# Optimization experiments

Measured on AMD Instinct MI355X. Metric: run time of the kernel, lower is better.

The kernel has to match this reference:

```python
import jax, jax.numpy as jnp
import numpy as np
import math

B, C, IMG, P = 256, 3, 32, 4
D, H = 256, 8
HD = D // H
T = (IMG // P) ** 2          # 64 patches
T1 = T + 1                   # +cls token
MLP_H = 2048
HEAD_H = T * D // 2          # 8192
NUM_CLASSES = 10
PATCH_DIM = C * P * P


def _pe(t1, d):
    pos = jnp.arange(t1, dtype=jnp.float32)[:, None]
    div = jnp.exp(jnp.arange(0, d, 2, dtype=jnp.float32) * (-math.log(10000.0) / d))
    s = jnp.sin(pos * div)   # [T1, d/2]
    c = jnp.cos(pos * div)
    return jnp.stack([s, c], axis=-1).reshape(t1, d)  # interleave: even=sin, odd=cos


def _ln2d(x, w, b, eps=1e-5):
    # LayerNorm over last two dims [T1, D] with affine params of shape [T1, D]
    mu = jnp.mean(x, axis=(-2, -1), keepdims=True)
    var = jnp.mean((x - mu) ** 2, axis=(-2, -1), keepdims=True)
    return (x - mu) * jax.lax.rsqrt(var + eps) * w + b


def setup_inputs() -> dict:
    key = jax.random.key(0)
    ks = jax.random.split(key, 16)
    s = 0.02
    inp = {
        "x": jax.random.normal(ks[0], (B, C, IMG, IMG), dtype=jnp.float32),
        "cls_token": jax.random.normal(ks[1], (1, 1, D), dtype=jnp.float32),
        "Wp": jax.random.normal(ks[2], (PATCH_DIM, D), dtype=jnp.float32) * s,
        "bp": jnp.zeros((D,), jnp.float32),
        # 2 transformer blocks, params stacked on leading axis
        "qkv_w": jax.random.normal(ks[3], (2, D, 3 * D), dtype=jnp.float32) * s,
        "qkv_b": jnp.zeros((2, 3 * D), jnp.float32),
        "ln_w": jnp.ones((2, T1, D), jnp.float32),
        "ln_b": jnp.zeros((2, T1, D), jnp.float32),
        "mlp1_w": jax.random.normal(ks[4], (2, D, MLP_H), dtype=jnp.float32) * s,
        "mlp1_b": jnp.zeros((2, MLP_H), jnp.float32),
        "mlp2_w": jax.random.normal(ks[5], (2, MLP_H, D), dtype=jnp.float32) * s,
        "mlp2_b": jnp.zeros((2, D), jnp.float32),
        "head1_w": jax.random.normal(ks[6], (T1 * D, HEAD_H), dtype=jnp.float32) * s,
        "head1_b": jnp.zeros((HEAD_H,), jnp.float32),
        "head2_w": jax.random.normal(ks[7], (HEAD_H, NUM_CLASSES), dtype=jnp.float32) * s,
        "head2_b": jnp.zeros((NUM_CLASSES,), jnp.float32),
    }
    return inp


def reference(x, cls_token, Wp, bp, qkv_w, qkv_b, ln_w, ln_b,
              mlp1_w, mlp1_b, mlp2_w, mlp2_b, head1_w, head1_b, head2_w, head2_b):
    b = x.shape[0]
    n = IMG // P
    # patchify: [B,C,n,P,n,P] -> [B,n,n,C,P,P] -> [B, T, C*P*P]  (C-major per patch)
    patches = x.reshape(b, C, n, P, n, P).transpose(0, 2, 4, 1, 3, 5).reshape(b, T, PATCH_DIM)
    out = patches @ Wp + bp                                     # [B, T, D]
    cls = jnp.broadcast_to(cls_token, (b, 1, D))
    out = jnp.concatenate([cls, out], axis=1)                   # [B, T1, D]
    out = out + _pe(T1, D)[None]

    scale = 1.0 / math.sqrt(HD)
    for i in range(2):  # dropout is eval-mode identity
        h = _ln2d(out, ln_w[i], ln_b[i])
        qkv = (h @ qkv_w[i] + qkv_b[i]).reshape(b, T1, H, 3, HD)
        q, k, v = qkv[..., 0, :], qkv[..., 1, :], qkv[..., 2, :]   # [B,S,H,hd]
        scores = jnp.einsum('bqhd,bkhd->bhqk', q, k) * scale
        a = jax.nn.softmax(scores, axis=-1)
        attn = jnp.einsum('bhqk,bkhd->bqhd', a, v).reshape(b, T1, D)
        r = attn + out
        h2 = _ln2d(r, ln_w[i], ln_b[i])                          # same LN reused
        m = jax.nn.relu(h2 @ mlp1_w[i] + mlp1_b[i])
        out = (m @ mlp2_w[i] + mlp2_b[i]) + r

    flat = out.reshape(b, T1 * D)
    hidden = jax.nn.silu(flat @ head1_w + head1_b)
    return hidden @ head2_w + head2_b                            # [B, 10] logits
```

## Files before the change

kernel.cpp:

```cpp
#include <hip/hip_runtime.h>
#include <hip/hip_fp16.h>
#include <math.h>
#include <stdint.h>

#define B_ 256
#define C_ 3
#define IMG_ 32
#define D_ 256
#define H_ 8
#define HD_ 32
#define T1_ 65
#define MLP_H_ 2048
#define HEAD_H_ 8192
#define NCLS 10
#define PDIM 48
#define M_ROWS (B_*T1_)

typedef _Float16 f16;
typedef _Float16 f16x8 __attribute__((ext_vector_type(8)));
typedef _Float16 f16x4 __attribute__((ext_vector_type(4)));
typedef float f32x4 __attribute__((ext_vector_type(4)));

typedef const void __attribute__((address_space(1))) glob_cv;
typedef void __attribute__((address_space(3))) lds_v;

__device__ __forceinline__ void async16(const void* g, void* l) {
    __builtin_amdgcn_global_load_lds((glob_cv*)g, (lds_v*)l, 16, 0, 0);
}

__global__ __launch_bounds__(256) void wpt_build(const float* __restrict__ Wp,
                                                 f16* __restrict__ WpT) {
    int idx = blockIdx.x * 256 + threadIdx.x;
    int d = idx >> 6, j = idx & 63;
    WpT[idx] = (j < PDIM) ? (f16)Wp[j * D_ + d] : (f16)0.f;
}

__global__ __launch_bounds__(256) void patch_mfma(
        const float* __restrict__ x, const float* __restrict__ cls,
        const f16* __restrict__ WpT, const float* __restrict__ bp,
        float* __restrict__ out) {
    int b = blockIdx.x;
    __shared__ float xs[3072];
    __shared__ __align__(16) f16 Ap[64 * 64];
    __shared__ __align__(16) f16 Bp[256 * 64];
    int tid = threadIdx.x;
    int lane = tid & 63, wid = tid >> 6;
    int lr = lane & 15, kq = lane >> 4;

    for (int i = tid; i < 768; i += 256)
        ((float4*)xs)[i] = ((const float4*)(x + (size_t)b * 3072))[i];
    for (int i = tid; i < 2048; i += 256)
        async16(WpT + (size_t)i * 8, &Bp[i * 8]);
    __syncthreads();
    for (int i = tid; i < 64 * 64; i += 256) {
        int t = i >> 6, j = i & 63;
        float val = 0.f;
        if (j < PDIM) {
            int py = t >> 3, px = t & 7;
            int c = j >> 4, rr = j & 15;
            int iy = rr >> 2, ix = rr & 3;
            val = xs[c * 1024 + (py * 4 + iy) * 32 + px * 4 + ix];
        }
        Ap[i] = (f16)val;
    }
    __syncthreads();

    for (int tile = wid; tile < 64; tile += 4) {
        int mi = tile >> 4, ni = tile & 15;
        f32x4 acc = {0.f, 0.f, 0.f, 0.f};
        #pragma unroll
        for (int ks = 0; ks < 2; ++ks) {
            f16x8 a = *(const f16x8*)&Ap[(mi * 16 + lr) * 64 + ks * 32 + kq * 8];
            f16x8 bb = *(const f16x8*)&Bp[(ni * 16 + lr) * 64 + ks * 32 + kq * 8];
            acc = __builtin_amdgcn_mfma_f32_16x16x32_f16(a, bb, acc, 0, 0, 0);
        }
        int d = ni * 16 + lr;
        float div = __expf((float)(d & ~1) * (-9.210340371976184f / 256.0f));
        #pragma unroll
        for (int r = 0; r < 4; ++r) {
            int t = 1 + mi * 16 + kq * 4 + r;
            float ang = (float)t * div;
            float pe = (d & 1) ? __cosf(ang) : __sinf(ang);
            out[((size_t)b * T1_ + t) * D_ + d] = acc[r] + bp[d] + pe;
        }
    }
    out[(size_t)b * T1_ * D_ + tid] = cls[tid] + ((tid & 1) ? 1.f : 0.f);
}

__global__ __launch_bounds__(1024) void ln_kernel(
        const float* __restrict__ xin, const float* __restrict__ w,
        const float* __restrict__ bb, f16* __restrict__ hout) {
    int b = blockIdx.x;
    const float4* x4 = (const float4*)(xin + (size_t)b * (T1_ * D_));
    const float4* w4 = (const float4*)w;
    const float4* b4 = (const float4*)bb;
    int tid = threadIdx.x;
    float s = 0.f, s2 = 0.f;
    for (int i = tid; i < 4160; i += 1024) {
        float4 v = x4[i];
        s  += v.x + v.y + v.z + v.w;
        s2 += v.x * v.x + v.y * v.y + v.z * v.z + v.w * v.w;
    }
    #pragma unroll
    for (int o = 32; o > 0; o >>= 1) { s += __shfl_down(s, o); s2 += __shfl_down(s2, o); }
    __shared__ float rs[16], rs2[16];
    __shared__ float mu_s, rstd_s;
    int wid = tid >> 6;
    if ((tid & 63) == 0) { rs[wid] = s; rs2[wid] = s2; }
    __syncthreads();
    if (tid == 0) {
        float S = 0.f, S2 = 0.f;
        #pragma unroll
        for (int i = 0; i < 16; ++i) { S += rs[i]; S2 += rs2[i]; }
        const float inv_n = 1.0f / (float)(T1_ * D_);
        float mu = S * inv_n;
        float var = S2 * inv_n - mu * mu;
        mu_s = mu; rstd_s = rsqrtf(var + 1e-5f);
    }
    __syncthreads();
    float mu = mu_s, rstd = rstd_s;
    f16* hb = hout + (size_t)b * (T1_ * D_);
    for (int i = tid; i < 4160; i += 1024) {
        float4 v = x4[i]; float4 wv = w4[i]; float4 bv = b4[i];
        f16x4 h;
        h[0] = (f16)((v.x - mu) * rstd * wv.x + bv.x);
        h[1] = (f16)((v.y - mu) * rstd * wv.y + bv.y);
        h[2] = (f16)((v.z - mu) * rstd * wv.z + bv.z);
        h[3] = (f16)((v.w - mu) * rstd * wv.w + bv.w);
        *(f16x4*)(hb + i * 4) = h;
    }
}

__global__ __launch_bounds__(256) void transpose_cvt(
        const float* __restrict__ W, f16* __restrict__ Wt, int K, int N) {
    __shared__ float L[32][33];
    int n0 = blockIdx.x * 32, k0 = blockIdx.y * 32;
    int t = threadIdx.x;
    int r = t >> 3, c4 = (t & 7) * 4;
    const float4 v = *(const float4*)(W + (size_t)(k0 + r) * N + n0 + c4);
    L[r][c4] = v.x; L[r][c4 + 1] = v.y; L[r][c4 + 2] = v.z; L[r][c4 + 3] = v.w;
    __syncthreads();
    f16x4 h;
    h[0] = (f16)L[c4][r]; h[1] = (f16)L[c4 + 1][r];
    h[2] = (f16)L[c4 + 2][r]; h[3] = (f16)L[c4 + 3][r];
    *(f16x4*)(Wt + (size_t)(n0 + r) * K + k0 + c4) = h;
}

template<int EPI, typename OutT>
__global__ __launch_bounds__(256) void gemm_f16(
        const f16* __restrict__ A, const f16* __restrict__ Bt,
        const float* __restrict__ bias, const float* __restrict__ Res,
        OutT* __restrict__ Cc, f16* __restrict__ C2, int M, int N, int K) {
    __shared__ __align__(16) f16 As[128 * 32];
    __shared__ __align__(16) f16 Bs[128 * 32];
    int nb = blockIdx.x, mb = blockIdx.y;
    int t = threadIdx.x;
    int lane = t & 63, wid = t >> 6;
    int wr = wid >> 1, wc = wid & 1;
    int lr = lane & 15, kq = lane >> 4;
    int row0 = mb * 128, col0 = nb * 128;

    f32x4 acc[4][4];
    #pragma unroll
    for (int mi = 0; mi < 4; ++mi)
        #pragma unroll
        for (int ni = 0; ni < 4; ++ni)
            #pragma unroll
            for (int r = 0; r < 4; ++r) acc[mi][ni][r] = 0.f;

    int sr = t >> 2;
    int k8 = (t & 3) * 8;
    const f16* Ab = A + (size_t)row0 * K + k8;
    const f16* Bb = Bt + (size_t)col0 * K + k8;

    for (int k0 = 0; k0 < K; k0 += 32) {
        __syncthreads();
        async16(Ab + (size_t)sr * K + k0,        &As[t * 8]);
        async16(Ab + (size_t)(sr + 64) * K + k0, &As[2048 + t * 8]);
        async16(Bb + (size_t)sr * K + k0,        &Bs[t * 8]);
        async16(Bb + (size_t)(sr + 64) * K + k0, &Bs[2048 + t * 8]);
        __syncthreads();
        f16x8 af[4], bf[4];
        #pragma unroll
        for (int mi = 0; mi < 4; ++mi)
            af[mi] = *(const f16x8*)&As[(wr * 64 + mi * 16 + lr) * 32 + kq * 8];
        #pragma unroll
        for (int ni = 0; ni < 4; ++ni)
            bf[ni] = *(const f16x8*)&Bs[(wc * 64 + ni * 16 + lr) * 32 + kq * 8];
        #pragma unroll
        for (int mi = 0; mi < 4; ++mi)
            #pragma unroll
            for (int ni = 0; ni < 4; ++ni)
                acc[mi][ni] = __builtin_amdgcn_mfma_f32_16x16x32_f16(af[mi], bf[ni], acc[mi][ni], 0, 0, 0);
    }

    #pragma unroll
    for (int mi = 0; mi < 4; ++mi) {
        #pragma unroll
        for (int ni = 0; ni < 4; ++ni) {
            int col = col0 + wc * 64 + ni * 16 + lr;
            #pragma unroll
            for (int r = 0; r < 4; ++r) {
                int row = row0 + wr * 64 + mi * 16 + kq * 4 + r;
                float v = acc[mi][ni][r] + bias[col];
                if (EPI == 1) v = fmaxf(v, 0.f);
                if (EPI == 2 || EPI == 3) v += Res[(size_t)row * N + col];
                Cc[(size_t)row * N + col] = (OutT)v;
                if (EPI == 3) C2[(size_t)row * N + col] = (f16)v;
            }
        }
    }
}

__global__ __launch_bounds__(256) void gemm_head1(
        const f16* __restrict__ A, const float* __restrict__ Bw,
        float* __restrict__ Cp) {
    __shared__ __align__(16) f16 As[256 * 32];
    __shared__ __align__(16) float Bs[32 * 64];
    const int K = M_ROWS, N = HEAD_H_;
    int nb = blockIdx.x;
    int z = blockIdx.y;
    int t = threadIdx.x;
    int lane = t & 63, wid = t >> 6;
    int lr = lane & 15, kq = lane >> 4;
    int col0 = nb * 64;
    int kstart = z * (K / 4);

    f32x4 acc[4][4];
    #pragma unroll
    for (int mi = 0; mi < 4; ++mi)
        #pragma unroll
        for (int ni = 0; ni < 4; ++ni)
            #pragma unroll
            for (int r = 0; r < 4; ++r) acc[mi][ni][r] = 0.f;

    int sr = t >> 2;
    int k8 = (t & 3) * 8;
    const f16* Ab = A + k8;
    int bkr = t >> 4;
    int bnc = (t & 15) * 4;
    const float* Bb = Bw + col0 + bnc;

    for (int k0 = kstart; k0 < kstart + K / 4; k0 += 32) {
        __syncthreads();
        #pragma unroll
        for (int r = 0; r < 4; ++r)
            async16(Ab + (size_t)(sr + r * 64) * K + k0, &As[r * 2048 + t * 8]);
        async16(Bb + (size_t)(k0 + bkr) * N,      &Bs[t * 4]);
        async16(Bb + (size_t)(k0 + 16 + bkr) * N, &Bs[1024 + t * 4]);
        __syncthreads();
        f16x8 af[4];
        #pragma unroll
        for (int mi = 0; mi < 4; ++mi)
            af[mi] = *(const f16x8*)&As[(wid * 64 + mi * 16 + lr) * 32 + kq * 8];
        #pragma unroll
        for (int ni = 0; ni < 4; ++ni) {
            f16x8 bf;
            #pragma unroll
            for (int j = 0; j < 8; ++j) bf[j] = (f16)Bs[(kq * 8 + j) * 64 + ni * 16 + lr];
            #pragma unroll
            for (int mi = 0; mi < 4; ++mi)
                acc[mi][ni] = __builtin_amdgcn_mfma_f32_16x16x32_f16(af[mi], bf, acc[mi][ni], 0, 0, 0);
        }
    }

    float* Cout = Cp + (size_t)z * 256 * N;
    #pragma unroll
    for (int mi = 0; mi < 4; ++mi) {
        #pragma unroll
        for (int ni = 0; ni < 4; ++ni) {
            int col = col0 + ni * 16 + lr;
            #pragma unroll
            for (int r = 0; r < 4; ++r) {
                int row = wid * 64 + mi * 16 + kq * 4 + r;
                Cout[(size_t)row * N + col] = acc[mi][ni][r];
            }
        }
    }
}

__global__ __launch_bounds__(256) void attn_kernel(
        const f16* __restrict__ qkv, const float* __restrict__ outres,
        float* __restrict__ r) {
    int b = blockIdx.x >> 3, h = blockIdx.x & 7;
    __shared__ __align__(16) f16 Qs[80 * 32];
    __shared__ __align__(16) f16 Ks[80 * 32];
    __shared__ __align__(16) f16 Vt[32 * 96];
    __shared__ float Sf[80 * 81];
    __shared__ __align__(16) f16 Pf[80 * 96];
    int tid = threadIdx.x;
    int lane = tid & 63, wid = tid >> 6;
    int lr = lane & 15, kq = lane >> 4;
    const float scale = 0.17677669529663687f;

    const f16* base = qkv + (size_t)b * T1_ * 768 + h * 96;
    for (int i = tid; i < T1_ * 12; i += 256) {
        int t = i / 12, c = i % 12;
        f16x8 vv = *(const f16x8*)(base + (size_t)t * 768 + c * 8);
        if (c < 4) {
            f16x8 q8;
            #pragma unroll
            for (int j = 0; j < 8; ++j) q8[j] = (f16)((float)vv[j] * scale);
            *(f16x8*)&Qs[t * 32 + c * 8] = q8;
        } else if (c < 8) {
            *(f16x8*)&Ks[t * 32 + (c - 4) * 8] = vv;
        } else {
            int d0 = (c - 8) * 8;
            #pragma unroll
            for (int j = 0; j < 8; ++j) Vt[(d0 + j) * 96 + t] = vv[j];
        }
    }
    for (int i = tid; i < 32 * 31; i += 256) {
        int d = i / 31, kt = 65 + i % 31;
        Vt[d * 96 + kt] = (f16)0.f;
    }
    __syncthreads();

    for (int tile = wid; tile < 25; tile += 4) {
        int mi = tile / 5, ni = tile % 5;
        f16x8 a = *(const f16x8*)&Qs[(mi * 16 + lr) * 32 + kq * 8];
        f16x8 bb = *(const f16x8*)&Ks[(ni * 16 + lr) * 32 + kq * 8];
        f32x4 c = {0.f, 0.f, 0.f, 0.f};
        c = __builtin_amdgcn_mfma_f32_16x16x32_f16(a, bb, c, 0, 0, 0);
        #pragma unroll
        for (int rr2 = 0; rr2 < 4; ++rr2)
            Sf[(mi * 16 + kq * 4 + rr2) * 81 + ni * 16 + lr] = c[rr2];
    }
    __syncthreads();

    for (int row = tid >> 2; row < T1_; row += 64) {
        int sub = tid & 3;
        float m = -1e30f;
        for (int kt = sub; kt < T1_; kt += 4) m = fmaxf(m, Sf[row * 81 + kt]);
        m = fmaxf(m, __shfl_xor(m, 1));
        m = fmaxf(m, __shfl_xor(m, 2));
        float sum = 0.f;
        for (int kt = sub; kt < T1_; kt += 4) {
            float e = __expf(Sf[row * 81 + kt] - m);
            Sf[row * 81 + kt] = e; sum += e;
        }
        sum += __shfl_xor(sum, 1);
        sum += __shfl_xor(sum, 2);
        float inv = 1.f / sum;
        for (int kt = sub; kt < T1_; kt += 4)
            Pf[row * 96 + kt] = (f16)(Sf[row * 81 + kt] * inv);
        for (int kt = T1_ + sub; kt < 96; kt += 4)
            Pf[row * 96 + kt] = (f16)0.f;
    }
    __syncthreads();

    for (int tile = wid; tile < 10; tile += 4) {
        int mi = tile >> 1, ni = tile & 1;
        f32x4 acc = {0.f, 0.f, 0.f, 0.f};
        #pragma unroll
        for (int ks = 0; ks < 3; ++ks) {
            f16x8 a = *(const f16x8*)&Pf[(mi * 16 + lr) * 96 + ks * 32 + kq * 8];
            f16x8 bv = *(const f16x8*)&Vt[(ni * 16 + lr) * 96 + ks * 32 + kq * 8];
            acc = __builtin_amdgcn_mfma_f32_16x16x32_f16(a, bv, acc, 0, 0, 0);
        }
        #pragma unroll
        for (int rr2 = 0; rr2 < 4; ++rr2) {
            int qt = mi * 16 + kq * 4 + rr2;
            if (qt < T1_) {
                size_t o = ((size_t)b * T1_ + qt) * D_ + h * HD_ + ni * 16 + lr;
                r[o] = acc[rr2] + outres[o];
            }
        }
    }
}

__global__ __launch_bounds__(256) void head2_fused(
        const float* __restrict__ part, const float* __restrict__ h1b,
        const float* __restrict__ w, const float* __restrict__ h2b,
        float* __restrict__ out) {
    int b = blockIdx.x;
    const int NP = 256 * HEAD_H_;
    int tid = threadIdx.x;
    float acc[NCLS];
    #pragma unroll
    for (int n = 0; n < NCLS; ++n) acc[n] = 0.f;
    for (int kk = tid; kk < HEAD_H_; kk += 256) {
        size_t o = (size_t)b * HEAD_H_ + kk;
        float v = part[o] + part[o + NP] + part[o + 2 * (size_t)NP] + part[o + 3 * (size_t)NP]
                + h1b[kk];
        v = v / (1.f + __expf(-v));
        const float* wr = w + (size_t)kk * NCLS;
        #pragma unroll
        for (int n = 0; n < NCLS; ++n) acc[n] += v * wr[n];
    }
    #pragma unroll
    for (int n = 0; n < NCLS; ++n)
        #pragma unroll
        for (int o = 32; o > 0; o >>= 1) acc[n] += __shfl_down(acc[n], o);
    __shared__ float red[4][NCLS];
    int wid = tid >> 6;
    if ((tid & 63) == 0)
        for (int n = 0; n < NCLS; ++n) red[wid][n] = acc[n];
    __syncthreads();
    if (tid < NCLS) {
        int n = tid;
        out[(size_t)b * NCLS + n] = red[0][n] + red[1][n] + red[2][n] + red[3][n] + h2b[n];
    }
}

extern "C" void kernel_launch(void* const* d_in, const int* in_sizes, int n_in,
                              void* d_out, int out_size, void* d_ws, size_t ws_size,
                              hipStream_t stream) {
    (void)in_sizes; (void)n_in; (void)out_size; (void)ws_size;
    const float* x       = (const float*)d_in[0];
    const float* cls     = (const float*)d_in[1];
    const float* Wp      = (const float*)d_in[2];
    const float* bp      = (const float*)d_in[3];
    const float* qkv_w   = (const float*)d_in[4];
    const float* qkv_b   = (const float*)d_in[5];
    const float* ln_w    = (const float*)d_in[6];
    const float* ln_b    = (const float*)d_in[7];
    const float* mlp1_w  = (const float*)d_in[8];
    const float* mlp1_b  = (const float*)d_in[9];
    const float* mlp2_w  = (const float*)d_in[10];
    const float* mlp2_b  = (const float*)d_in[11];
    const float* head1_w = (const float*)d_in[12];
    const float* head1_b = (const float*)d_in[13];
    const float* head2_w = (const float*)d_in[14];
    const float* head2_b = (const float*)d_in[15];
    float* outp = (float*)d_out;

    char* ws = (char*)d_ws;
    size_t off = 0;
    auto alloc = [&](size_t bytes) -> void* {
        void* p = ws + off; off += (bytes + 255) & ~(size_t)255; return p;
    };
    float* s_out = (float*)alloc((size_t)M_ROWS * D_ * 4);
    float* s_r   = (float*)alloc((size_t)M_ROWS * D_ * 4);
    f16*   s_h   = (f16*)  alloc((size_t)M_ROWS * D_ * 2);
    void*  s_big = alloc((size_t)M_ROWS * MLP_H_ * 2);
    f16*   w_qkv_t  = (f16*)alloc((size_t)2 * 768 * 256 * 2);
    f16*   w_mlp1_t = (f16*)alloc((size_t)2 * 2048 * 256 * 2);
    f16*   w_mlp2_t = (f16*)alloc((size_t)2 * 256 * 2048 * 2);
    f16*   wpT      = (f16*)alloc((size_t)256 * 64 * 2);
    f16*   s_flat   = s_h;
    f16*   s_qkv = (f16*)s_big;
    f16*   s_m   = (f16*)s_big;
    float* s_part = (float*)s_big;

    dim3 blk(256);

    for (int i = 0; i < 2; ++i) {
        transpose_cvt<<<dim3(768 / 32, 256 / 32), blk, 0, stream>>>(
            qkv_w + (size_t)i * D_ * 768, w_qkv_t + (size_t)i * 768 * 256, 256, 768);
        transpose_cvt<<<dim3(2048 / 32, 256 / 32), blk, 0, stream>>>(
            mlp1_w + (size_t)i * D_ * 2048, w_mlp1_t + (size_t)i * 2048 * 256, 256, 2048);
        transpose_cvt<<<dim3(256 / 32, 2048 / 32), blk, 0, stream>>>(
            mlp2_w + (size_t)i * 2048 * 256, w_mlp2_t + (size_t)i * 256 * 2048, 2048, 256);
    }
    wpt_build<<<dim3(64), blk, 0, stream>>>(Wp, wpT);
    patch_mfma<<<dim3(B_), blk, 0, stream>>>(x, cls, wpT, bp, s_out);

    for (int i = 0; i < 2; ++i) {
        const float* lw = ln_w + (size_t)i * T1_ * D_;
        const float* lb = ln_b + (size_t)i * T1_ * D_;
        ln_kernel<<<dim3(B_), dim3(1024), 0, stream>>>(s_out, lw, lb, s_h);
        gemm_f16<0, f16><<<dim3(768 / 128, M_ROWS / 128), blk, 0, stream>>>(
            s_h, w_qkv_t + (size_t)i * 768 * 256, qkv_b + (size_t)i * 768,
            nullptr, s_qkv, nullptr, M_ROWS, 768, 256);
        attn_kernel<<<dim3(B_ * H_), blk, 0, stream>>>(s_qkv, s_out, s_r);
        ln_kernel<<<dim3(B_), dim3(1024), 0, stream>>>(s_r, lw, lb, s_h);
        gemm_f16<1, f16><<<dim3(MLP_H_ / 128, M_ROWS / 128), blk, 0, stream>>>(
            s_h, w_mlp1_t + (size_t)i * 2048 * 256, mlp1_b + (size_t)i * MLP_H_,
            nullptr, s_m, nullptr, M_ROWS, MLP_H_, 256);
        if (i == 0) {
            gemm_f16<2, float><<<dim3(D_ / 128, M_ROWS / 128), blk, 0, stream>>>(
                s_m, w_mlp2_t + (size_t)i * 256 * 2048, mlp2_b + (size_t)i * D_,
                s_r, s_out, nullptr, M_ROWS, D_, MLP_H_);
        } else {
            gemm_f16<3, float><<<dim3(D_ / 128, M_ROWS / 128), blk, 0, stream>>>(
                s_m, w_mlp2_t + (size_t)i * 256 * 2048, mlp2_b + (size_t)i * D_,
                s_r, s_out, s_flat, M_ROWS, D_, MLP_H_);
        }
    }

    gemm_head1<<<dim3(HEAD_H_ / 64, 4), blk, 0, stream>>>(s_flat, head1_w, s_part);
    head2_fused<<<dim3(B_), blk, 0, stream>>>(s_part, head1_b, head2_w, head2_b, outp);
}
```

Before: 1.153 ms.

## Double-buffer GEMM LDS tiles, convert head1 weights to f16 in LDS, merge weight prep

The generic f16 GEMM and the head1 GEMM now double-buffer their LDS tiles, so the next K-slice is prefetched while MFMAs run on the current one. This removes one barrier per iteration. In head1 the fp32 weight tile is loaded into registers, converted to f16 and stored transposed into a swizzled LDS layout, replacing eight scalar strided LDS reads plus conversions per fragment. The seven weight transpose/convert launches and the Wp build are merged into a single prep kernel to cut launch overhead. The cost is doubled LDS use, which may lower occupancy, and more register pressure from the prefetched B values.

```diff
diff --git a/kernel.cpp b/kernel.cpp
--- a/kernel.cpp
+++ b/kernel.cpp
@@ -19,6 +19,7 @@
 typedef _Float16 f16;
 typedef _Float16 f16x8 __attribute__((ext_vector_type(8)));
 typedef _Float16 f16x4 __attribute__((ext_vector_type(4)));
+typedef _Float16 f16x2 __attribute__((ext_vector_type(2)));
 typedef float f32x4 __attribute__((ext_vector_type(4)));
 
 typedef const void __attribute__((address_space(1))) glob_cv;
@@ -28,11 +29,44 @@
     __builtin_amdgcn_global_load_lds((glob_cv*)g, (lds_v*)l, 16, 0, 0);
 }
 
-__global__ __launch_bounds__(256) void wpt_build(const float* __restrict__ Wp,
-                                                 f16* __restrict__ WpT) {
-    int idx = blockIdx.x * 256 + threadIdx.x;
-    int d = idx >> 6, j = idx & 63;
-    WpT[idx] = (j < PDIM) ? (f16)Wp[j * D_ + d] : (f16)0.f;
+__global__ __launch_bounds__(256) void prep_weights(
+        const float* __restrict__ qkv_w, const float* __restrict__ mlp1_w,
+        const float* __restrict__ mlp2_w, const float* __restrict__ Wp,
+        f16* __restrict__ w_qkv_t, f16* __restrict__ w_mlp1_t,
+        f16* __restrict__ w_mlp2_t, f16* __restrict__ wpT) {
+    int id = blockIdx.x;
+    if (id >= 2432) {
+        int idx = (id - 2432) * 256 + threadIdx.x;
+        int d = idx >> 6, j = idx & 63;
+        wpT[idx] = (j < PDIM) ? (f16)Wp[j * D_ + d] : (f16)0.f;
+        return;
+    }
+    const float* W; f16* Wt; int K, N, nbx, rel;
+    if (id < 384) {
+        int L = id >= 192; rel = id - L * 192;
+        W = qkv_w + (size_t)L * D_ * 768; Wt = w_qkv_t + (size_t)L * 768 * 256;
+        K = 256; N = 768; nbx = 24;
+    } else if (id < 1408) {
+        int L = (id - 384) >= 512; rel = (id - 384) - L * 512;
+        W = mlp1_w + (size_t)L * D_ * 2048; Wt = w_mlp1_t + (size_t)L * 2048 * 256;
+        K = 256; N = 2048; nbx = 64;
+    } else {
+        int L = (id - 1408) >= 512; rel = (id - 1408) - L * 512;
+        W = mlp2_w + (size_t)L * 2048 * 256; Wt = w_mlp2_t + (size_t)L * 256 * 2048;
+        K = 2048; N = 256; nbx = 8;
+    }
+    int bx = rel % nbx, by = rel / nbx;
+    int n0 = bx * 32, k0 = by * 32;
+    __shared__ float L2d[32][33];
+    int t = threadIdx.x;
+    int r = t >> 3, c4 = (t & 7) * 4;
+    const float4 v = *(const float4*)(W + (size_t)(k0 + r) * N + n0 + c4);
+    L2d[r][c4] = v.x; L2d[r][c4 + 1] = v.y; L2d[r][c4 + 2] = v.z; L2d[r][c4 + 3] = v.w;
+    __syncthreads();
+    f16x4 h;
+    h[0] = (f16)L2d[c4][r]; h[1] = (f16)L2d[c4 + 1][r];
+    h[2] = (f16)L2d[c4 + 2][r]; h[3] = (f16)L2d[c4 + 3][r];
+    *(f16x4*)(Wt + (size_t)(n0 + r) * K + k0 + c4) = h;
 }
 
 __global__ __launch_bounds__(256) void patch_mfma(
@@ -131,28 +165,13 @@
     }
 }
 
-__global__ __launch_bounds__(256) void transpose_cvt(
-        const float* __restrict__ W, f16* __restrict__ Wt, int K, int N) {
-    __shared__ float L[32][33];
-    int n0 = blockIdx.x * 32, k0 = blockIdx.y * 32;
-    int t = threadIdx.x;
-    int r = t >> 3, c4 = (t & 7) * 4;
-    const float4 v = *(const float4*)(W + (size_t)(k0 + r) * N + n0 + c4);
-    L[r][c4] = v.x; L[r][c4 + 1] = v.y; L[r][c4 + 2] = v.z; L[r][c4 + 3] = v.w;
-    __syncthreads();
-    f16x4 h;
-    h[0] = (f16)L[c4][r]; h[1] = (f16)L[c4 + 1][r];
-    h[2] = (f16)L[c4 + 2][r]; h[3] = (f16)L[c4 + 3][r];
-    *(f16x4*)(Wt + (size_t)(n0 + r) * K + k0 + c4) = h;
-}
-
 template<int EPI, typename OutT>
 __global__ __launch_bounds__(256) void gemm_f16(
         const f16* __restrict__ A, const f16* __restrict__ Bt,
         const float* __restrict__ bias, const float* __restrict__ Res,
         OutT* __restrict__ Cc, f16* __restrict__ C2, int M, int N, int K) {
-    __shared__ __align__(16) f16 As[128 * 32];
-    __shared__ __align__(16) f16 Bs[128 * 32];
+    __shared__ __align__(16) f16 As[2][128 * 32];
+    __shared__ __align__(16) f16 Bs[2][128 * 32];
     int nb = blockIdx.x, mb = blockIdx.y;
     int t = threadIdx.x;
     int lane = t & 63, wid = t >> 6;
@@ -173,25 +192,35 @@
     const f16* Ab = A + (size_t)row0 * K + k8;
     const f16* Bb = Bt + (size_t)col0 * K + k8;
 
+    async16(Ab + (size_t)sr * K,        &As[0][t * 8]);
+    async16(Ab + (size_t)(sr + 64) * K, &As[0][2048 + t * 8]);
+    async16(Bb + (size_t)sr * K,        &Bs[0][t * 8]);
+    async16(Bb + (size_t)(sr + 64) * K, &Bs[0][2048 + t * 8]);
+    __syncthreads();
+
+    int cur = 0;
     for (int k0 = 0; k0 < K; k0 += 32) {
-        __syncthreads();
-        async16(Ab + (size_t)sr * K + k0,        &As[t * 8]);
-        async16(Ab + (size_t)(sr + 64) * K + k0, &As[2048 + t * 8]);
-        async16(Bb + (size_t)sr * K + k0,        &Bs[t * 8]);
-        async16(Bb + (size_t)(sr + 64) * K + k0, &Bs[2048 + t * 8]);
-        __syncthreads();
+        int nxt = cur ^ 1;
+        if (k0 + 32 < K) {
+            async16(Ab + (size_t)sr * K + k0 + 32,        &As[nxt][t * 8]);
+            async16(Ab + (size_t)(sr + 64) * K + k0 + 32, &As[nxt][2048 + t * 8]);
+            async16(Bb + (size_t)sr * K + k0 + 32,        &Bs[nxt][t * 8]);
+            async16(Bb + (size_t)(sr + 64) * K + k0 + 32, &Bs[nxt][2048 + t * 8]);
+        }
         f16x8 af[4], bf[4];
         #pragma unroll
         for (int mi = 0; mi < 4; ++mi)
-            af[mi] = *(const f16x8*)&As[(wr * 64 + mi * 16 + lr) * 32 + kq * 8];
+            af[mi] = *(const f16x8*)&As[cur][(wr * 64 + mi * 16 + lr) * 32 + kq * 8];
         #pragma unroll
         for (int ni = 0; ni < 4; ++ni)
-            bf[ni] = *(const f16x8*)&Bs[(wc * 64 + ni * 16 + lr) * 32 + kq * 8];
+            bf[ni] = *(const f16x8*)&Bs[cur][(wc * 64 + ni * 16 + lr) * 32 + kq * 8];
         #pragma unroll
         for (int mi = 0; mi < 4; ++mi)
             #pragma unroll
             for (int ni = 0; ni < 4; ++ni)
                 acc[mi][ni] = __builtin_amdgcn_mfma_f32_16x16x32_f16(af[mi], bf[ni], acc[mi][ni], 0, 0, 0);
+        __syncthreads();
+        cur = nxt;
     }
 
     #pragma unroll
@@ -212,11 +241,15 @@
     }
 }
 
+__device__ __forceinline__ int bswz(int col, int k) {
+    return col * 32 + (k ^ (((col >> 2) & 3) << 3));
+}
+
 __global__ __launch_bounds__(256) void gemm_head1(
         const f16* __restrict__ A, const float* __restrict__ Bw,
         float* __restrict__ Cp) {
-    __shared__ __align__(16) f16 As[256 * 32];
-    __shared__ __align__(16) float Bs[32 * 64];
+    __shared__ __align__(16) f16 As[2][256 * 32];
+    __shared__ __align__(16) f16 Bs[2][64 * 32];
     const int K = M_ROWS, N = HEAD_H_;
     int nb = blockIdx.x;
     int z = blockIdx.y;
@@ -225,6 +258,7 @@
     int lr = lane & 15, kq = lane >> 4;
     int col0 = nb * 64;
     int kstart = z * (K / 4);
+    int kend = kstart + K / 4;
 
     f32x4 acc[4][4];
     #pragma unroll
@@ -237,31 +271,57 @@
     int sr = t >> 2;
     int k8 = (t & 3) * 8;
     const f16* Ab = A + k8;
-    int bkr = t >> 4;
-    int bnc = (t & 15) * 4;
-    const float* Bb = Bw + col0 + bnc;
-
-    for (int k0 = kstart; k0 < kstart + K / 4; k0 += 32) {
+    int kp = (t >> 4) * 2;
+    int c0 = (t & 15) * 4;
+    const float* Bb = Bw + col0 + c0;
+
+    f32x4 bv0, bv1;
+
+    auto stageA = [&](int buf, int k0) {
+        #pragma unroll
+        for (int r = 0; r < 4; ++r)
+            async16(Ab + (size_t)(sr + r * 64) * K + k0, &As[buf][r * 2048 + t * 8]);
+    };
+    auto loadB = [&](int k0) {
+        bv0 = *(const f32x4*)(Bb + (size_t)(k0 + kp) * N);
+        bv1 = *(const f32x4*)(Bb + (size_t)(k0 + kp + 1) * N);
+    };
+    auto writeB = [&](int buf) {
+        #pragma unroll
+        for (int c = 0; c < 4; ++c) {
+            f16x2 hv; hv[0] = (f16)bv0[c]; hv[1] = (f16)bv1[c];
+            *(f16x2*)&Bs[buf][bswz(c0 + c, kp)] = hv;
+        }
+    };
+
+    stageA(0, kstart);
+    loadB(kstart);
+    writeB(0);
+    __syncthreads();
+
+    int cur = 0;
+    for (int k0 = kstart; k0 < kend; k0 += 32) {
+        int nxt = cur ^ 1;
+        bool pre = (k0 + 32 < kend);
+        if (pre) {
+            loadB(k0 + 32);
+            stageA(nxt, k0 + 32);
+        }
+        f16x8 af[4], bf[4];
+        #pragma unroll
+        for (int mi = 0; mi < 4; ++mi)
+            af[mi] = *(const f16x8*)&As[cur][(wid * 64 + mi * 16 + lr) * 32 + kq * 8];
+        #pragma unroll
+        for (int ni = 0; ni < 4; ++ni)
+            bf[ni] = *(const f16x8*)&Bs[cur][bswz(ni * 16 + lr, kq * 8)];
+        #pragma unroll
+        for (int mi = 0; mi < 4; ++mi)
+            #pragma unroll
+            for (int ni = 0; ni < 4; ++ni)
+                acc[mi][ni] = __builtin_amdgcn_mfma_f32_16x16x32_f16(af[mi], bf[ni], acc[mi][ni], 0, 0, 0);
+        if (pre) writeB(nxt);
         __syncthreads();
-        #pragma unroll
-        for (int r = 0; r < 4; ++r)
-            async16(Ab + (size_t)(sr + r * 64) * K + k0, &As[r * 2048 + t * 8]);
-        async16(Bb + (size_t)(k0 + bkr) * N,      &Bs[t * 4]);
-        async16(Bb + (size_t)(k0 + 16 + bkr) * N, &Bs[1024 + t * 4]);
-        __syncthreads();
-        f16x8 af[4];
-        #pragma unroll
-        for (int mi = 0; mi < 4; ++mi)
-            af[mi] = *(const f16x8*)&As[(wid * 64 + mi * 16 + lr) * 32 + kq * 8];
-        #pragma unroll
-        for (int ni = 0; ni < 4; ++ni) {
-            f16x8 bf;
-            #pragma unroll
-            for (int j = 0; j < 8; ++j) bf[j] = (f16)Bs[(kq * 8 + j) * 64 + ni * 16 + lr];
-            #pragma unroll
-            for (int mi = 0; mi < 4; ++mi)
-                acc[mi][ni] = __builtin_amdgcn_mfma_f32_16x16x32_f16(af[mi], bf, acc[mi][ni], 0, 0, 0);
-        }
+        cur = nxt;
     }
 
     float* Cout = Cp + (size_t)z * 256 * N;
@@ -445,15 +505,8 @@
 
     dim3 blk(256);
 
-    for (int i = 0; i < 2; ++i) {
-        transpose_cvt<<<dim3(768 / 32, 256 / 32), blk, 0, stream>>>(
-            qkv_w + (size_t)i * D_ * 768, w_qkv_t + (size_t)i * 768 * 256, 256, 768);
-        transpose_cvt<<<dim3(2048 / 32, 256 / 32), blk, 0, stream>>>(
-            mlp1_w + (size_t)i * D_ * 2048, w_mlp1_t + (size_t)i * 2048 * 256, 256, 2048);
-        transpose_cvt<<<dim3(256 / 32, 2048 / 32), blk, 0, stream>>>(
-            mlp2_w + (size_t)i * 2048 * 256, w_mlp2_t + (size_t)i * 256 * 2048, 2048, 256);
-    }
-    wpt_build<<<dim3(64), blk, 0, stream>>>(Wp, wpT);
+    prep_weights<<<dim3(2496), blk, 0, stream>>>(
+        qkv_w, mlp1_w, mlp2_w, Wp, w_qkv_t, w_mlp1_t, w_mlp2_t, wpT);
     patch_mfma<<<dim3(B_), blk, 0, stream>>>(x, cls, wpT, bp, s_out);
 
     for (int i = 0; i < 2; ++i) {
```

Result: faster. 1.117 ms (-3.1%).
